# Optimization experiments

Hardware: AMD Instinct MI355X
Metric: run time of the kernel (lower is better)

Reference implementation:

```python
import jax, jax.numpy as jnp
import numpy as np

EPS = 1e-16


def setup_inputs() -> dict:
    key = jax.random.key(0)
    k1, k2 = jax.random.split(key)
    N, D = 512, 4096
    a = jax.random.normal(k1, (N, D), dtype=jnp.float32)
    p = jax.random.normal(k2, (N, D), dtype=jnp.float32)
    return {"a": a, "p": p}


def reference(a, p):
    N = a.shape[0]
    # Pairwise squared distances between anchors a and positives p:
    # ||a_i||^2 - 2 a_i . p_j + ||p_j||^2   (diag(a a^T) == row norms)
    dot = jnp.matmul(a, p.T)                       # [N, N]
    sq_a = jnp.sum(a * a, axis=-1)                 # [N]
    sq_p = jnp.sum(p * p, axis=-1)                 # [N]
    d2 = sq_a[:, None] - 2.0 * dot + sq_p[None, :]
    d2 = jnp.maximum(d2, 0.0)                      # distances[distances < 0] = 0
    zero_mask = (d2 == 0.0).astype(d2.dtype)
    dist = (1.0 - zero_mask) * jnp.sqrt(d2 + zero_mask * EPS)  # [N, N]

    # Triplet tensor: loss[a, p, n] = dist[a, p] - dist[a, n]
    triplet = dist[:, :, None] - dist[:, None, :]  # [N, N, N]

    # Validity mask: labels = arange(N) -> valid iff p == anchor and n != anchor
    labels = jnp.arange(N)
    label_eq = labels[:, None] == labels[None, :]  # [N, N]
    mask = label_eq[:, :, None] & (~label_eq[:, None, :])  # [N, N, N]

    triplet = mask.astype(triplet.dtype) * triplet
    triplet = jax.nn.relu(triplet)

    num_positive = jnp.sum(triplet > EPS).astype(triplet.dtype)
    loss = jnp.sum(triplet) / (num_positive + EPS)
    return loss
```

## Files before the change

kernel.cpp:

```cpp
#include <hip/hip_runtime.h>
#include <math.h>

#define PN 512
#define PD 4096

#define BK 256
#define NST (PD / BK)

#define WS_AH_BYTES 8192
#define WS_PH_BYTES (8192 + 4194304)
#define WS_NEED_MAIN ((size_t)(8192 + 2 * 4194304))

typedef __attribute__((ext_vector_type(8))) short short8;
typedef __attribute__((ext_vector_type(4))) float floatx4;

static __device__ __forceinline__ unsigned short f2bf(float x) {
    unsigned int u = __float_as_uint(x);
    u += 0x7fffu + ((u >> 16) & 1u);
    return (unsigned short)(u >> 16);
}

static __device__ __forceinline__ void load16_lds(const void* gp, void* lp) {
    __builtin_amdgcn_global_load_lds(
        (const __attribute__((address_space(1))) unsigned int*)gp,
        (__attribute__((address_space(3))) unsigned int*)lp,
        16, 0, 0);
}

struct ushort4s { unsigned short x, y, z, w; };

__global__ __launch_bounds__(256) void taw_prep_kernel(
        const float* __restrict__ a, const float* __restrict__ p,
        float* __restrict__ ws, int conv) {
    const int i = blockIdx.x;
    const int t = threadIdx.x;
    if (i == 0 && t == 0) {
        ws[1536] = 0.0f;
        ((unsigned int*)ws)[1537] = 0u;
        ((unsigned int*)ws)[1538] = 0u;
    }
    const float4* a4 = (const float4*)(a + (size_t)i * PD);
    const float4* p4 = (const float4*)(p + (size_t)i * PD);
    unsigned short* ah = (unsigned short*)((char*)ws + WS_AH_BYTES) + (size_t)i * PD;
    unsigned short* ph = (unsigned short*)((char*)ws + WS_PH_BYTES) + (size_t)i * PD;
    float sa = 0.f, sp = 0.f, dp = 0.f;
#pragma unroll
    for (int c = 0; c < 4; ++c) {
        const int e = c * 256 + t;
        float4 av = a4[e];
        float4 pv = p4[e];
        sa += av.x * av.x + av.y * av.y + av.z * av.z + av.w * av.w;
        sp += pv.x * pv.x + pv.y * pv.y + pv.z * pv.z + pv.w * pv.w;
        dp += av.x * pv.x + av.y * pv.y + av.z * pv.z + av.w * pv.w;
        if (conv) {
            ushort4s ab = {f2bf(av.x), f2bf(av.y), f2bf(av.z), f2bf(av.w)};
            ushort4s pb = {f2bf(pv.x), f2bf(pv.y), f2bf(pv.z), f2bf(pv.w)};
            *(ushort4s*)(ah + (size_t)e * 4) = ab;
            *(ushort4s*)(ph + (size_t)e * 4) = pb;
        }
    }
#pragma unroll
    for (int off = 32; off > 0; off >>= 1) {
        sa += __shfl_down(sa, off, 64);
        sp += __shfl_down(sp, off, 64);
        dp += __shfl_down(dp, off, 64);
    }
    __shared__ float red[3][4];
    const int wave = t >> 6;
    if ((t & 63) == 0) { red[0][wave] = sa; red[1][wave] = sp; red[2][wave] = dp; }
    __syncthreads();
    if (t == 0) {
        sa = red[0][0] + red[0][1] + red[0][2] + red[0][3];
        sp = red[1][0] + red[1][1] + red[1][2] + red[1][3];
        dp = red[2][0] + red[2][1] + red[2][2] + red[2][3];
        float d2 = sa - 2.f * dp + sp;
        d2 = fmaxf(d2, 0.f);
        ws[i] = sa;
        ws[512 + i] = sp;
        ws[1024 + i] = (d2 == 0.f) ? 0.f : sqrtf(d2);
    }
}

__global__ __launch_bounds__(256) void taw_fused_kernel(
        float* __restrict__ ws, float* __restrict__ out) {
    __shared__ short lds[3][32][64][8];
    const unsigned short* ah = (const unsigned short*)((const char*)ws + WS_AH_BYTES);
    const unsigned short* ph = (const unsigned short*)((const char*)ws + WS_PH_BYTES);
    const int t = threadIdx.x;
    const int lane = t & 63;
    const int w = t >> 6;

    const int B = blockIdx.x;
    const int xcd = B & 7;
    const int l = B >> 3;
    const int bi = ((xcd >> 1) << 2) + (l >> 3);
    const int bj = ((xcd & 1) << 3) + (l & 7);
    const int i0 = bi * 32;
    const int j0 = bj * 32;

    const unsigned short* sbase[8];
#pragma unroll
    for (int q = 0; q < 8; ++q) {
        const int g16 = w * 8 + q;
        const int g = g16 & 15;
        const int row = ((g & 1) << 4) + (lane & 15);
        const int kk = ((g >> 1) << 5) + ((lane >> 4) << 3);
        sbase[q] = (g16 < 16 ? ah + (size_t)(i0 + row) * PD
                             : ph + (size_t)(j0 + row) * PD) + kk;
    }

    auto STAGE = [&](int buf, int kst) {
#pragma unroll
        for (int q = 0; q < 8; ++q) {
            load16_lds(sbase[q] + kst, &lds[buf][w * 8 + q][0][0]);
        }
    };

    floatx4 acc[2][2];
#pragma unroll
    for (int rm = 0; rm < 2; ++rm)
#pragma unroll
        for (int rn = 0; rn < 2; ++rn) acc[rm][rn] = (floatx4){0.f, 0.f, 0.f, 0.f};

    STAGE(0, 0);
    STAGE(1, BK);
    for (int st = 0; st < NST; ++st) {
        const int b = st - (st / 3) * 3;
        if (st + 2 < NST) {
            STAGE(st + 2 - ((st + 2) / 3) * 3, (st + 2) * BK);
            asm volatile("s_waitcnt vmcnt(16)" ::: "memory");
        } else if (st + 1 < NST) {
            asm volatile("s_waitcnt vmcnt(8)" ::: "memory");
        } else {
            asm volatile("s_waitcnt vmcnt(0)" ::: "memory");
        }
        __builtin_amdgcn_s_barrier();
        __builtin_amdgcn_sched_barrier(0);
#pragma unroll
        for (int c = 0; c < 2; ++c) {
            const int kb = 2 * w + c;
            short8 a0 = *(const short8*)&lds[b][2 * kb + 0][lane][0];
            short8 a1 = *(const short8*)&lds[b][2 * kb + 1][lane][0];
            short8 p0 = *(const short8*)&lds[b][16 + 2 * kb + 0][lane][0];
            short8 p1 = *(const short8*)&lds[b][16 + 2 * kb + 1][lane][0];
            acc[0][0] = __builtin_amdgcn_mfma_f32_16x16x32_bf16(a0, p0, acc[0][0], 0, 0, 0);
            acc[0][1] = __builtin_amdgcn_mfma_f32_16x16x32_bf16(a0, p1, acc[0][1], 0, 0, 0);
            acc[1][0] = __builtin_amdgcn_mfma_f32_16x16x32_bf16(a1, p0, acc[1][0], 0, 0, 0);
            acc[1][1] = __builtin_amdgcn_mfma_f32_16x16x32_bf16(a1, p1, acc[1][1], 0, 0, 0);
        }
        __builtin_amdgcn_sched_barrier(0);
        asm volatile("s_waitcnt lgkmcnt(0)" ::: "memory");
        __builtin_amdgcn_s_barrier();
    }

    float* sc = (float*)&lds[0][0][0][0];
#pragma unroll
    for (int rm = 0; rm < 2; ++rm)
#pragma unroll
        for (int rn = 0; rn < 2; ++rn)
#pragma unroll
            for (int r = 0; r < 4; ++r)
                sc[(((w * 2 + rm) * 2 + rn) * 4 + r) * 64 + lane] = acc[rm][rn][r];
    __syncthreads();

    const int rm = w >> 1, rn = w & 1;
    const int jj = j0 + rn * 16 + (lane & 15);
    const int ib = i0 + rm * 16 + ((lane >> 4) << 2);
    const float spv = ws[512 + jj];
    float lsum = 0.f;
    unsigned int lcnt = 0;
#pragma unroll
    for (int r = 0; r < 4; ++r) {
        const float dot = sc[(((0 * 2 + rm) * 2 + rn) * 4 + r) * 64 + lane]
                        + sc[(((1 * 2 + rm) * 2 + rn) * 4 + r) * 64 + lane]
                        + sc[(((2 * 2 + rm) * 2 + rn) * 4 + r) * 64 + lane]
                        + sc[(((3 * 2 + rm) * 2 + rn) * 4 + r) * 64 + lane];
        const int ii = ib + r;
        float d2 = ws[ii] - 2.f * dot + spv;
        d2 = fmaxf(d2, 0.f);
        const float dist = (d2 == 0.f) ? 0.f : sqrtf(d2);
        const float v = (ii != jj) ? fmaxf(ws[1024 + ii] - dist, 0.f) : 0.f;
        lsum += v;
        lcnt += (v > 1e-16f) ? 1u : 0u;
    }
#pragma unroll
    for (int off = 32; off > 0; off >>= 1) {
        lsum += __shfl_down(lsum, off, 64);
        lcnt += __shfl_down(lcnt, off, 64);
    }
    float* rs = sc + 4096;
    unsigned int* rc = (unsigned int*)(sc + 4100);
    if ((t & 63) == 0) { rs[w] = lsum; rc[w] = lcnt; }
    __syncthreads();
    if (t == 0) {
        atomicAdd(ws + 1536, rs[0] + rs[1] + rs[2] + rs[3]);
        atomicAdd(((unsigned int*)ws) + 1537, rc[0] + rc[1] + rc[2] + rc[3]);
        __threadfence();
        const unsigned int old = atomicAdd(((unsigned int*)ws) + 1538, 1u);
        if (old == 255u) {
            const float s = atomicAdd(ws + 1536, 0.f);
            const unsigned int c = atomicAdd(((unsigned int*)ws) + 1537, 0u);
            out[0] = (float)((double)s / ((double)c + 1e-16));
        }
    }
}

__global__ void taw_finalize_kernel(const float* __restrict__ ws,
                                    float* __restrict__ out) {
    const double s = (double)ws[1536];
    const double c = (double)(((const unsigned int*)ws)[1537]);
    out[0] = (float)(s / (c + 1e-16));
}

__global__ __launch_bounds__(256) void taw_gemm_loss_kernel(
        const float* __restrict__ A, const float* __restrict__ P,
        float* __restrict__ ws) {
    __shared__ float as[32][34];
    __shared__ float bs[32][34];
    const int tx = threadIdx.x;
    const int ty = threadIdx.y;
    const int t = ty * 16 + tx;
    const int i0 = blockIdx.y * 32;
    const int j0 = blockIdx.x * 32;
    const int sr = t >> 3;
    const int sk = (t & 7) * 4;
    const float* aptr = A + (size_t)(i0 + sr) * PD + sk;
    const float* pptr = P + (size_t)(j0 + sr) * PD + sk;
    float c00 = 0.f, c01 = 0.f, c10 = 0.f, c11 = 0.f;
    for (int k0 = 0; k0 < PD; k0 += 32) {
        float4 av = *(const float4*)(aptr + k0);
        float4 pv = *(const float4*)(pptr + k0);
        __syncthreads();
        as[sk + 0][sr] = av.x; as[sk + 1][sr] = av.y;
        as[sk + 2][sr] = av.z; as[sk + 3][sr] = av.w;
        bs[sk + 0][sr] = pv.x; bs[sk + 1][sr] = pv.y;
        bs[sk + 2][sr] = pv.z; bs[sk + 3][sr] = pv.w;
        __syncthreads();
#pragma unroll
        for (int kk = 0; kk < 32; ++kk) {
            const float2 a2 = *(const float2*)&as[kk][2 * ty];
            const float2 b2 = *(const float2*)&bs[kk][2 * tx];
            c00 = fmaf(a2.x, b2.x, c00);
            c01 = fmaf(a2.x, b2.y, c01);
            c10 = fmaf(a2.y, b2.x, c10);
            c11 = fmaf(a2.y, b2.y, c11);
        }
    }
    const float* sq_a = ws;
    const float* sq_p = ws + 512;
    const float* ddg  = ws + 1024;
    const int i = i0 + 2 * ty;
    const int j = j0 + 2 * tx;
    float cvals[2][2] = {{c00, c01}, {c10, c11}};
    float lsum = 0.f;
    unsigned int lcnt = 0;
#pragma unroll
    for (int dr = 0; dr < 2; ++dr)
#pragma unroll
        for (int dc = 0; dc < 2; ++dc) {
            const int ii = i + dr, jj = j + dc;
            float d2 = sq_a[ii] - 2.f * cvals[dr][dc] + sq_p[jj];
            d2 = fmaxf(d2, 0.f);
            const float dist = (d2 == 0.f) ? 0.f : sqrtf(d2);
            const float v = (ii != jj) ? fmaxf(ddg[ii] - dist, 0.f) : 0.f;
            lsum += v;
            lcnt += (v > 1e-16f) ? 1u : 0u;
        }
#pragma unroll
    for (int off = 32; off > 0; off >>= 1) {
        lsum += __shfl_down(lsum, off, 64);
        lcnt += __shfl_down(lcnt, off, 64);
    }
    __shared__ float rsum[4];
    __shared__ unsigned int rcnt[4];
    if ((t & 63) == 0) { rsum[t >> 6] = lsum; rcnt[t >> 6] = lcnt; }
    __syncthreads();
    if (t == 0) {
        atomicAdd(ws + 1536, rsum[0] + rsum[1] + rsum[2] + rsum[3]);
        atomicAdd(((unsigned int*)ws) + 1537, rcnt[0] + rcnt[1] + rcnt[2] + rcnt[3]);
    }
}

extern "C" void kernel_launch(void* const* d_in, const int* in_sizes, int n_in,
                              void* d_out, int out_size, void* d_ws, size_t ws_size,
                              hipStream_t stream) {
    (void)in_sizes; (void)n_in; (void)out_size;
    const float* a = (const float*)d_in[0];
    const float* p = (const float*)d_in[1];
    float* out = (float*)d_out;
    float* ws = (float*)d_ws;

    const int use_mfma = (ws_size >= WS_NEED_MAIN) ? 1 : 0;
    taw_prep_kernel<<<PN, 256, 0, stream>>>(a, p, ws, use_mfma);
    if (use_mfma) {
        taw_fused_kernel<<<256, 256, 0, stream>>>(ws, out);
    } else {
        taw_gemm_loss_kernel<<<dim3(16, 16), dim3(16, 16), 0, stream>>>(a, p, ws);
        taw_finalize_kernel<<<1, 1, 0, stream>>>(ws, out);
    }
}
```

Baseline: 94.35 us.

## Shrink fused GEMM tile to 32x16 and launch 512 blocks

The fused bf16 MFMA GEMM+loss kernel now uses 32x16 output tiles instead of 32x32, so the launch grows from 256 to 512 blocks and covers more of the CUs. Each wave now issues 2 MFMAs per k-chunk instead of 4. Per-block LDS staging drops from 8 to 6 loads per thread per stage, and the wait counts and the last-block completion counter are adjusted to match. The cost is more total global traffic, because each A tile is now reloaded for twice as many column blocks, and lower MFMA work per LDS load.

New measurement: 106.8 us. +13.2%, slower.

```diff
diff --git a/kernel.cpp b/kernel.cpp
--- a/kernel.cpp
+++ b/kernel.cpp
@@ -83,7 +83,7 @@
 
 __global__ __launch_bounds__(256) void taw_fused_kernel(
         float* __restrict__ ws, float* __restrict__ out) {
-    __shared__ short lds[3][32][64][8];
+    __shared__ short lds[3][24][64][8];
     const unsigned short* ah = (const unsigned short*)((const char*)ws + WS_AH_BYTES);
     const unsigned short* ph = (const unsigned short*)((const char*)ws + WS_PH_BYTES);
     const int t = threadIdx.x;
@@ -93,34 +93,40 @@
     const int B = blockIdx.x;
     const int xcd = B & 7;
     const int l = B >> 3;
-    const int bi = ((xcd >> 1) << 2) + (l >> 3);
-    const int bj = ((xcd & 1) << 3) + (l & 7);
+    const int bi = ((xcd >> 1) << 2) + (l >> 4);
+    const int bj = ((xcd & 1) << 4) + (l & 15);
     const int i0 = bi * 32;
-    const int j0 = bj * 32;
-
-    const unsigned short* sbase[8];
-#pragma unroll
-    for (int q = 0; q < 8; ++q) {
-        const int g16 = w * 8 + q;
-        const int g = g16 & 15;
-        const int row = ((g & 1) << 4) + (lane & 15);
-        const int kk = ((g >> 1) << 5) + ((lane >> 4) << 3);
-        sbase[q] = (g16 < 16 ? ah + (size_t)(i0 + row) * PD
-                             : ph + (size_t)(j0 + row) * PD) + kk;
+    const int j0 = bj * 16;
+
+    const unsigned short* sbase[6];
+#pragma unroll
+    for (int q = 0; q < 6; ++q) {
+        const int G = w * 6 + q;
+        const unsigned short* bp;
+        int row, kk;
+        if (G < 16) {
+            row = i0 + ((G & 1) << 4) + (lane & 15);
+            kk = ((G >> 1) << 5) + ((lane >> 4) << 3);
+            bp = ah;
+        } else {
+            const int g = G - 16;
+            row = j0 + (lane & 15);
+            kk = (g << 5) + ((lane >> 4) << 3);
+            bp = ph;
+        }
+        sbase[q] = bp + (size_t)row * PD + kk;
     }
 
     auto STAGE = [&](int buf, int kst) {
 #pragma unroll
-        for (int q = 0; q < 8; ++q) {
-            load16_lds(sbase[q] + kst, &lds[buf][w * 8 + q][0][0]);
+        for (int q = 0; q < 6; ++q) {
+            load16_lds(sbase[q] + kst, &lds[buf][w * 6 + q][0][0]);
         }
     };
 
-    floatx4 acc[2][2];
-#pragma unroll
-    for (int rm = 0; rm < 2; ++rm)
-#pragma unroll
-        for (int rn = 0; rn < 2; ++rn) acc[rm][rn] = (floatx4){0.f, 0.f, 0.f, 0.f};
+    floatx4 acc[2];
+    acc[0] = (floatx4){0.f, 0.f, 0.f, 0.f};
+    acc[1] = (floatx4){0.f, 0.f, 0.f, 0.f};
 
     STAGE(0, 0);
     STAGE(1, BK);
@@ -128,9 +134,9 @@
         const int b = st - (st / 3) * 3;
         if (st + 2 < NST) {
             STAGE(st + 2 - ((st + 2) / 3) * 3, (st + 2) * BK);
-            asm volatile("s_waitcnt vmcnt(16)" ::: "memory");
+            asm volatile("s_waitcnt vmcnt(12)" ::: "memory");
         } else if (st + 1 < NST) {
-            asm volatile("s_waitcnt vmcnt(8)" ::: "memory");
+            asm volatile("s_waitcnt vmcnt(6)" ::: "memory");
         } else {
             asm volatile("s_waitcnt vmcnt(0)" ::: "memory");
         }
@@ -141,12 +147,9 @@
             const int kb = 2 * w + c;
             short8 a0 = *(const short8*)&lds[b][2 * kb + 0][lane][0];
             short8 a1 = *(const short8*)&lds[b][2 * kb + 1][lane][0];
-            short8 p0 = *(const short8*)&lds[b][16 + 2 * kb + 0][lane][0];
-            short8 p1 = *(const short8*)&lds[b][16 + 2 * kb + 1][lane][0];
-            acc[0][0] = __builtin_amdgcn_mfma_f32_16x16x32_bf16(a0, p0, acc[0][0], 0, 0, 0);
-            acc[0][1] = __builtin_amdgcn_mfma_f32_16x16x32_bf16(a0, p1, acc[0][1], 0, 0, 0);
-            acc[1][0] = __builtin_amdgcn_mfma_f32_16x16x32_bf16(a1, p0, acc[1][0], 0, 0, 0);
-            acc[1][1] = __builtin_amdgcn_mfma_f32_16x16x32_bf16(a1, p1, acc[1][1], 0, 0, 0);
+            short8 p0 = *(const short8*)&lds[b][16 + kb][lane][0];
+            acc[0] = __builtin_amdgcn_mfma_f32_16x16x32_bf16(a0, p0, acc[0], 0, 0, 0);
+            acc[1] = __builtin_amdgcn_mfma_f32_16x16x32_bf16(a1, p0, acc[1], 0, 0, 0);
         }
         __builtin_amdgcn_sched_barrier(0);
         asm volatile("s_waitcnt lgkmcnt(0)" ::: "memory");
@@ -157,47 +160,47 @@
 #pragma unroll
     for (int rm = 0; rm < 2; ++rm)
 #pragma unroll
-        for (int rn = 0; rn < 2; ++rn)
-#pragma unroll
-            for (int r = 0; r < 4; ++r)
-                sc[(((w * 2 + rm) * 2 + rn) * 4 + r) * 64 + lane] = acc[rm][rn][r];
+        for (int r = 0; r < 4; ++r)
+            sc[((w * 2 + rm) * 4 + r) * 64 + lane] = acc[rm][r];
     __syncthreads();
 
-    const int rm = w >> 1, rn = w & 1;
-    const int jj = j0 + rn * 16 + (lane & 15);
-    const int ib = i0 + rm * 16 + ((lane >> 4) << 2);
-    const float spv = ws[512 + jj];
     float lsum = 0.f;
     unsigned int lcnt = 0;
-#pragma unroll
-    for (int r = 0; r < 4; ++r) {
-        const float dot = sc[(((0 * 2 + rm) * 2 + rn) * 4 + r) * 64 + lane]
-                        + sc[(((1 * 2 + rm) * 2 + rn) * 4 + r) * 64 + lane]
-                        + sc[(((2 * 2 + rm) * 2 + rn) * 4 + r) * 64 + lane]
-                        + sc[(((3 * 2 + rm) * 2 + rn) * 4 + r) * 64 + lane];
-        const int ii = ib + r;
-        float d2 = ws[ii] - 2.f * dot + spv;
-        d2 = fmaxf(d2, 0.f);
-        const float dist = (d2 == 0.f) ? 0.f : sqrtf(d2);
-        const float v = (ii != jj) ? fmaxf(ws[1024 + ii] - dist, 0.f) : 0.f;
-        lsum += v;
-        lcnt += (v > 1e-16f) ? 1u : 0u;
-    }
-#pragma unroll
-    for (int off = 32; off > 0; off >>= 1) {
-        lsum += __shfl_down(lsum, off, 64);
-        lcnt += __shfl_down(lcnt, off, 64);
-    }
-    float* rs = sc + 4096;
-    unsigned int* rc = (unsigned int*)(sc + 4100);
-    if ((t & 63) == 0) { rs[w] = lsum; rc[w] = lcnt; }
+    if (w < 2) {
+        const int rm = w;
+        const int jj = j0 + (lane & 15);
+        const int ib = i0 + rm * 16 + ((lane >> 4) << 2);
+        const float spv = ws[512 + jj];
+#pragma unroll
+        for (int r = 0; r < 4; ++r) {
+            const float dot = sc[((0 * 2 + rm) * 4 + r) * 64 + lane]
+                            + sc[((1 * 2 + rm) * 4 + r) * 64 + lane]
+                            + sc[((2 * 2 + rm) * 4 + r) * 64 + lane]
+                            + sc[((3 * 2 + rm) * 4 + r) * 64 + lane];
+            const int ii = ib + r;
+            float d2 = ws[ii] - 2.f * dot + spv;
+            d2 = fmaxf(d2, 0.f);
+            const float dist = (d2 == 0.f) ? 0.f : sqrtf(d2);
+            const float v = (ii != jj) ? fmaxf(ws[1024 + ii] - dist, 0.f) : 0.f;
+            lsum += v;
+            lcnt += (v > 1e-16f) ? 1u : 0u;
+        }
+#pragma unroll
+        for (int off = 32; off > 0; off >>= 1) {
+            lsum += __shfl_down(lsum, off, 64);
+            lcnt += __shfl_down(lcnt, off, 64);
+        }
+    }
+    float* rs = sc + 2048;
+    unsigned int* rc = (unsigned int*)(sc + 2052);
+    if (w < 2 && lane == 0) { rs[w] = lsum; rc[w] = lcnt; }
     __syncthreads();
     if (t == 0) {
-        atomicAdd(ws + 1536, rs[0] + rs[1] + rs[2] + rs[3]);
-        atomicAdd(((unsigned int*)ws) + 1537, rc[0] + rc[1] + rc[2] + rc[3]);
+        atomicAdd(ws + 1536, rs[0] + rs[1]);
+        atomicAdd(((unsigned int*)ws) + 1537, rc[0] + rc[1]);
         __threadfence();
         const unsigned int old = atomicAdd(((unsigned int*)ws) + 1538, 1u);
-        if (old == 255u) {
+        if (old == 511u) {
             const float s = atomicAdd(ws + 1536, 0.f);
             const unsigned int c = atomicAdd(((unsigned int*)ws) + 1537, 0u);
             out[0] = (float)((double)s / ((double)c + 1e-16));
@@ -293,7 +296,7 @@
     const int use_mfma = (ws_size >= WS_NEED_MAIN) ? 1 : 0;
     taw_prep_kernel<<<PN, 256, 0, stream>>>(a, p, ws, use_mfma);
     if (use_mfma) {
-        taw_fused_kernel<<<256, 256, 0, stream>>>(ws, out);
+        taw_fused_kernel<<<512, 256, 0, stream>>>(ws, out);
     } else {
         taw_gemm_loss_kernel<<<dim3(16, 16), dim3(16, 16), 0, stream>>>(a, p, ws);
         taw_finalize_kernel<<<1, 1, 0, stream>>>(ws, out);
```
